# Kernel optimization log

Measured on AMD Instinct MI355X. Metric: run time of the kernel, lower is better.

## Reference

```python
import jax, jax.numpy as jnp
import numpy as np

B, T, C = 4, 2048, 2048
N_HEAD = 16
HEAD_DIM = C // N_HEAD
ROPE_BASE = 10000.0


def setup_inputs() -> dict:
    key = jax.random.key(0)
    k1, k2, k3 = jax.random.split(key, 3)
    x = jax.random.normal(k1, (B, T, C), dtype=jnp.float32)
    Wqkv = jax.random.normal(k2, (C, 3 * C), dtype=jnp.float32) * 0.02
    bqkv = jnp.zeros((3 * C,), dtype=jnp.float32)
    Wproj = jax.random.normal(k3, (C, C), dtype=jnp.float32) * 0.02
    bproj = jnp.zeros((C,), dtype=jnp.float32)
    return {"x": x, "Wqkv": Wqkv, "bqkv": bqkv, "Wproj": Wproj, "bproj": bproj}


def _rope_cos_sin(seq_len, head_dim, dtype):
    inv_freq = 1.0 / (ROPE_BASE ** (jnp.arange(0, head_dim, 2, dtype=jnp.float32) / head_dim))
    t = jnp.arange(seq_len, dtype=jnp.float32)
    freqs = jnp.einsum("i,j->ij", t, inv_freq)          # [T, D/2]
    emb = jnp.concatenate([freqs, freqs], axis=-1)       # [T, D]
    return jnp.cos(emb).astype(dtype), jnp.sin(emb).astype(dtype)


def _rotate_half(x):
    half = x.shape[-1] // 2
    x1, x2 = x[..., :half], x[..., half:]
    return jnp.concatenate([-x2, x1], axis=-1)


def reference(x, Wqkv, bqkv, Wproj, bproj):
    b, t, c = x.shape
    qkv = x @ Wqkv + bqkv                                # [B, T, 3C]
    q, k, v = jnp.split(qkv, 3, axis=-1)
    # [B, T, C] -> [B, H, T, D]
    def to_heads(u):
        return u.reshape(b, t, N_HEAD, HEAD_DIM).transpose(0, 2, 1, 3)
    q, k, v = to_heads(q), to_heads(k), to_heads(v)
    cos, sin = _rope_cos_sin(t, HEAD_DIM, x.dtype)       # [T, D]
    cos = cos[None, None]                                # [1, 1, T, D]
    sin = sin[None, None]
    q = q * cos + _rotate_half(q) * sin
    k = k * cos + _rotate_half(k) * sin
    scale = 1.0 / np.sqrt(HEAD_DIM).astype(np.float32)
    scores = jnp.einsum("bhqd,bhkd->bhqk", q, k) * scale  # [B, H, T, T]
    causal = jnp.tril(jnp.ones((t, t), dtype=bool))
    scores = jnp.where(causal[None, None], scores, jnp.finfo(scores.dtype).min)
    att = jax.nn.softmax(scores, axis=-1)
    y = jnp.einsum("bhqk,bhkd->bhqd", att, v)             # [B, H, T, D]
    y = y.transpose(0, 2, 1, 3).reshape(b, t, c)
    return y @ Wproj + bproj
```

## Files before the change

### kernel.cpp

```cpp
#include <hip/hip_runtime.h>
#include <hip/hip_bf16.h>
#include <stdint.h>
#include <math.h>

#define NB 4
#define NT 2048
#define NC 2048
#define NH 16
#define HD 128
#define BT (NB*NT)

typedef __attribute__((ext_vector_type(8))) short s16x8;
typedef __attribute__((ext_vector_type(4))) short s16x4;
typedef __attribute__((ext_vector_type(4))) float f32x4;

typedef __attribute__((address_space(1))) void as1_void;
typedef __attribute__((address_space(3))) void as3_void;

static __device__ __forceinline__ unsigned short f2bf(float f) {
  union { float f; uint32_t u; } v; v.f = f;
  return (unsigned short)((v.u + 0x7fffu + ((v.u >> 16) & 1u)) >> 16);
}
static __device__ __forceinline__ float bf2f(unsigned short u) {
  union { uint32_t u; float f; } v; v.u = ((uint32_t)u) << 16;
  return v.f;
}
static __device__ __forceinline__ void async16(unsigned short* lds, const unsigned short* g) {
  __builtin_amdgcn_global_load_lds((as1_void*)g, (as3_void*)lds, 16, 0, 0);
}
static __device__ __forceinline__ uint32_t lds_off(void* p) {
  return (uint32_t)(size_t)(as3_void*)p;
}

__global__ void k_convert_bf16(const float* __restrict__ in, unsigned short* __restrict__ out, int n8) {
  int i = blockIdx.x * blockDim.x + threadIdx.x;
  if (i >= n8) return;
  const float4* p = (const float4*)in + (size_t)i * 2;
  float4 a = p[0], b = p[1];
  union { unsigned short s[8]; uint4 u; } o;
  o.s[0] = f2bf(a.x); o.s[1] = f2bf(a.y); o.s[2] = f2bf(a.z); o.s[3] = f2bf(a.w);
  o.s[4] = f2bf(b.x); o.s[5] = f2bf(b.y); o.s[6] = f2bf(b.z); o.s[7] = f2bf(b.w);
  ((uint4*)out)[i] = o.u;
}

__global__ void k_transpose_bf16(const float* __restrict__ W, unsigned short* __restrict__ WT, int K, int N) {
  __shared__ unsigned short tile[64][65];
  const int k0 = blockIdx.y * 64, n0 = blockIdx.x * 64;
  const int t = threadIdx.x;
  const int jj = t & 63, base_i = t >> 6;
  #pragma unroll
  for (int p = 0; p < 16; ++p) {
    int i = p * 4 + base_i;
    tile[i][jj] = f2bf(W[(size_t)(k0 + i) * N + n0 + jj]);
  }
  __syncthreads();
  #pragma unroll
  for (int p = 0; p < 16; ++p) {
    int j = p * 4 + base_i;
    WT[(size_t)(n0 + j) * K + k0 + jj] = tile[jj][j];
  }
}

__global__ void k_rope(unsigned short* __restrict__ Q, unsigned short* __restrict__ Kb) {
  int idx = blockIdx.x * 256 + threadIdx.x;
  int g = idx & 7;
  int tpos = (idx >> 3) & (NT - 1);
  int bh = idx >> 14;
  size_t o = ((size_t)bh * NT + tpos) * HD + g * 8;
  s16x8 qlo = *(const s16x8*)(Q + o),  qhi = *(const s16x8*)(Q + o + 64);
  s16x8 klo = *(const s16x8*)(Kb + o), khi = *(const s16x8*)(Kb + o + 64);
  s16x8 oql, oqh, okl, okh;
  const float qs = 0.08838834764831845f * 1.4426950408889634f;
  #pragma unroll
  for (int e = 0; e < 8; ++e) {
    const int d = g * 8 + e;
    float invf = exp2f(-(float)d * 0.2076205059304602f);
    float ang = (float)tpos * invf;
    float s, c;
    __sincosf(ang, &s, &c);
    float q1 = bf2f((unsigned short)qlo[e]), q2 = bf2f((unsigned short)qhi[e]);
    float k1 = bf2f((unsigned short)klo[e]), k2 = bf2f((unsigned short)khi[e]);
    oql[e] = (short)f2bf((q1 * c - q2 * s) * qs);
    oqh[e] = (short)f2bf((q2 * c + q1 * s) * qs);
    okl[e] = (short)f2bf(k1 * c - k2 * s);
    okh[e] = (short)f2bf(k2 * c + k1 * s);
  }
  *(s16x8*)(Q + o)       = oql;
  *(s16x8*)(Q + o + 64)  = oqh;
  *(s16x8*)(Kb + o)      = okl;
  *(s16x8*)(Kb + o + 64) = okh;
}

template<int MODE>
__global__ __launch_bounds__(256, 2)
void k_gemm_bt2(const unsigned short* __restrict__ A,
                const unsigned short* __restrict__ Bt,
                const float* __restrict__ bias,
                float* __restrict__ OutF,
                unsigned short* __restrict__ Qd,
                unsigned short* __restrict__ Kd,
                unsigned short* __restrict__ Vd,
                int M, int N, int K)
{
  __shared__ __align__(16) unsigned short Al[256 * 64];
  __shared__ __align__(16) unsigned short Bl[128 * 64];
  const int t = threadIdx.x;
  const int l = t & 63;
  const int wv = t >> 6;
  const int wm = wv >> 1, wn = wv & 1;
  const int bm = blockIdx.y * 256, bn = blockIdx.x * 128;
  const int lr = l & 15, lg = l >> 4;

  f32x4 acc[8][4];
  #pragma unroll
  for (int i = 0; i < 8; ++i)
    #pragma unroll
    for (int j = 0; j < 4; ++j)
      acc[i][j] = f32x4{0.f, 0.f, 0.f, 0.f};

  for (int k0 = 0; k0 < K; k0 += 64) {
    #pragma unroll
    for (int i = 0; i < 8; ++i) {
      const int Cc = i * 256 + t;
      const int row = Cc >> 3;
      const int kc = (Cc & 7) ^ (row & 7);
      async16(&Al[(i * 256 + (t & 192)) * 8], &A[(size_t)(bm + row) * K + k0 + kc * 8]);
    }
    #pragma unroll
    for (int i = 0; i < 4; ++i) {
      const int Cc = i * 256 + t;
      const int row = Cc >> 3;
      const int kc = (Cc & 7) ^ (row & 7);
      async16(&Bl[(i * 256 + (t & 192)) * 8], &Bt[(size_t)(bn + row) * K + k0 + kc * 8]);
    }
    __syncthreads();
    #pragma unroll
    for (int kk = 0; kk < 2; ++kk) {
      s16x8 af[8], bfr[4];
      #pragma unroll
      for (int mi = 0; mi < 8; ++mi) {
        const int row = wm * 128 + mi * 16 + lr;
        const int ch = (kk * 4 + lg) ^ (row & 7);
        af[mi] = *(const s16x8*)&Al[row * 64 + ch * 8];
      }
      #pragma unroll
      for (int ni = 0; ni < 4; ++ni) {
        const int row = wn * 64 + ni * 16 + lr;
        const int ch = (kk * 4 + lg) ^ (row & 7);
        bfr[ni] = *(const s16x8*)&Bl[row * 64 + ch * 8];
      }
      __builtin_amdgcn_s_setprio(1);
      #pragma unroll
      for (int mi = 0; mi < 8; ++mi)
        #pragma unroll
        for (int ni = 0; ni < 4; ++ni)
          acc[mi][ni] = __builtin_amdgcn_mfma_f32_16x16x32_bf16(af[mi], bfr[ni], acc[mi][ni], 0, 0, 0);
      __builtin_amdgcn_s_setprio(0);
    }
    __syncthreads();
  }

  #pragma unroll
  for (int mi = 0; mi < 8; ++mi) {
    #pragma unroll
    for (int ni = 0; ni < 4; ++ni) {
      const int col = bn + wn * 64 + ni * 16 + lr;
      const float bv = bias[col];
      #pragma unroll
      for (int r = 0; r < 4; ++r) {
        const int row = bm + wm * 128 + mi * 16 + lg * 4 + r;
        const float v = acc[mi][ni][r] + bv;
        if (MODE == 1) {
          OutF[(size_t)row * N + col] = v;
        } else {
          const int which = col >> 11;
          const int cc = col & 2047;
          const int h = cc >> 7, d = cc & 127;
          const int b = row >> 11, tp = row & 2047;
          unsigned short* dst = (which == 0) ? Qd : (which == 1 ? Kd : Vd);
          dst[(((size_t)(b * NH + h)) * NT + tp) * HD + d] = f2bf(v);
        }
      }
    }
  }
}

__global__ __launch_bounds__(256, 2)
void k_attn(const unsigned short* __restrict__ Q,
            const unsigned short* __restrict__ Kg,
            const unsigned short* __restrict__ Vg,
            unsigned short* __restrict__ Yatt)
{
  __shared__ __align__(16) unsigned short Kl[2][64 * 128];
  __shared__ __align__(16) unsigned short Vl[2][64 * 128];
  const int bh = blockIdx.x;
  const int pair = blockIdx.y;
  const int b = bh >> 4, h = bh & 15;
  const int t = threadIdx.x, l = t & 63, wv = t >> 6;
  const int lr = l & 15, lg = l >> 4;
  const size_t hoff = (size_t)bh * NT * HD;
  const unsigned short* Qh = Q + hoff;
  const unsigned short* Kh = Kg + hoff;
  const unsigned short* Vh = Vg + hoff;
  const uint32_t vbase0 = lds_off(&Vl[0][0]);

  auto stageKV = [&](int buf, int kv0) {
    #pragma unroll
    for (int i = 0; i < 4; ++i) {
      const int Cc = i * 256 + t;
      {
        const int krow = Cc >> 4;
        const int kc = (Cc & 15) ^ (krow & 7);
        async16(&Kl[buf][(i * 256 + (t & 192)) * 8], &Kh[(size_t)(kv0 + krow) * HD + kc * 8]);
      }
      {
        const int S = Cc >> 3, c8 = Cc & 7;
        const int kq = S >> 3, dq = S & 7;
        const int vk = kq * 4 + (c8 >> 1), vd = dq * 16 + (c8 & 1) * 8;
        async16(&Vl[buf][(i * 256 + (t & 192)) * 8], &Vh[(size_t)(kv0 + vk) * HD + vd]);
      }
    }
  };

  #pragma unroll 1
  for (int rep = 0; rep < 2; ++rep) {
    const int qb = rep ? (31 - pair) : pair;
    const int q0w = qb * 64 + wv * 16;
    const int qrow = q0w + lr;

    __syncthreads();

    s16x8 qf[4];
    #pragma unroll
    for (int m = 0; m < 4; ++m)
      qf[m] = *(const s16x8*)(Qh + (size_t)qrow * HD + m * 32 + lg * 8);

    f32x4 yt[8];
    #pragma unroll
    for (int n = 0; n < 8; ++n) yt[n] = f32x4{0.f, 0.f, 0.f, 0.f};
    float mrun = -1e30f, lrun = 0.f;

    auto computeTile = [&](int buf, int kv0) {
      f32x4 st[4];
      __builtin_amdgcn_s_setprio(1);
      #pragma unroll
      for (int kt = 0; kt < 4; ++kt) {
        f32x4 a = f32x4{0.f, 0.f, 0.f, 0.f};
        const int krow = kt * 16 + lr;
        #pragma unroll
        for (int m = 0; m < 4; ++m) {
          const int ch = (m * 4 + lg) ^ (krow & 7);
          s16x8 kf = *(const s16x8*)&Kl[buf][krow * 128 + ch * 8];
          a = __builtin_amdgcn_mfma_f32_16x16x32_bf16(kf, qf[m], a, 0, 0, 0);
        }
        st[kt] = a;
      }
      __builtin_amdgcn_s_setprio(0);

      if (kv0 + 63 > q0w) {
        #pragma unroll
        for (int kt = 0; kt < 4; ++kt)
          #pragma unroll
          for (int r = 0; r < 4; ++r) {
            const int key = kv0 + kt * 16 + lg * 4 + r;
            if (key > qrow) st[kt][r] = -3.0e38f;
          }
      }

      float tm = -3.0e38f;
      #pragma unroll
      for (int kt = 0; kt < 4; ++kt)
        #pragma unroll
        for (int r = 0; r < 4; ++r) tm = fmaxf(tm, st[kt][r]);
      tm = fmaxf(tm, __shfl_xor(tm, 16));
      tm = fmaxf(tm, __shfl_xor(tm, 32));
      if (!__all(tm - mrun <= 8.0f)) {
        const float mnew = fmaxf(mrun, tm);
        const float fsc = exp2f(mrun - mnew);
        mrun = mnew;
        lrun *= fsc;
        #pragma unroll
        for (int n = 0; n < 8; ++n)
          #pragma unroll
          for (int r = 0; r < 4; ++r) yt[n][r] *= fsc;
      }

      float pv[16];
      float psum = 0.f;
      #pragma unroll
      for (int kt = 0; kt < 4; ++kt)
        #pragma unroll
        for (int r = 0; r < 4; ++r) {
          const float p = exp2f(st[kt][r] - mrun);
          psum += p;
          pv[kt * 4 + r] = p;
        }
      lrun += psum;

      union { uint32_t w[4]; s16x8 v; } pu[2];
      #pragma unroll
      for (int gk = 0; gk < 2; ++gk)
        #pragma unroll
        for (int w = 0; w < 4; ++w) {
          const int i0 = (gk * 2 + (w >> 1)) * 4 + (w & 1) * 2;
          asm("v_cvt_pk_bf16_f32 %0, %1, %2" : "=v"(pu[gk].w[w]) : "v"(pv[i0]), "v"(pv[i0 + 1]));
        }

      const uint32_t vb = vbase0 + (uint32_t)buf * 16384;
      #pragma unroll
      for (int gk = 0; gk < 2; ++gk) {
        s16x4 va[8], vb2[8];
        #pragma unroll
        for (int n = 0; n < 8; ++n) {
          const uint32_t a0 = vb + ((uint32_t)((gk * 8 + lg) * 8 + n)) * 128 + (uint32_t)lr * 8;
          asm volatile("ds_read_b64_tr_b16 %0, %1" : "=v"(va[n])  : "v"(a0));
          asm volatile("ds_read_b64_tr_b16 %0, %1" : "=v"(vb2[n]) : "v"(a0 + 4096));
        }
        asm volatile("s_waitcnt lgkmcnt(0)" ::: "memory");
        __builtin_amdgcn_sched_barrier(0);
        __builtin_amdgcn_s_setprio(1);
        #pragma unroll
        for (int n = 0; n < 8; ++n) {
          s16x8 vf;
          vf[0] = va[n][0];  vf[1] = va[n][1];  vf[2] = va[n][2];  vf[3] = va[n][3];
          vf[4] = vb2[n][0]; vf[5] = vb2[n][1]; vf[6] = vb2[n][2]; vf[7] = vb2[n][3];
          yt[n] = __builtin_amdgcn_mfma_f32_16x16x32_bf16(vf, pu[gk].v, yt[n], 0, 0, 0);
        }
        __builtin_amdgcn_s_setprio(0);
      }
    };

    const int nkv = qb + 1;
    stageKV(0, 0);
    asm volatile("s_waitcnt vmcnt(0)" ::: "memory");
    __syncthreads();
    int buf = 0;
    #pragma unroll 1
    for (int kv = 0; kv < nkv - 1; ++kv) {
      stageKV(buf ^ 1, (kv + 1) * 64);
      computeTile(buf, kv * 64);
      asm volatile("s_waitcnt vmcnt(0)" ::: "memory");
      __builtin_amdgcn_s_barrier();
      buf ^= 1;
    }
    computeTile(buf, (nkv - 1) * 64);

    lrun += __shfl_xor(lrun, 16);
    lrun += __shfl_xor(lrun, 32);
    const float inv = 1.f / lrun;
    unsigned short* yrow = Yatt + (size_t)(b * NT + q0w + lr) * NC + h * HD;
    #pragma unroll
    for (int n = 0; n < 8; ++n)
      #pragma unroll
      for (int r = 0; r < 4; ++r)
        yrow[n * 16 + lg * 4 + r] = f2bf(yt[n][r] * inv);
  }
}

extern "C" void kernel_launch(void* const* d_in, const int* in_sizes, int n_in,
                              void* d_out, int out_size, void* d_ws, size_t ws_size,
                              hipStream_t stream) {
  (void)in_sizes; (void)n_in; (void)out_size; (void)ws_size;
  const float* x     = (const float*)d_in[0];
  const float* Wqkv  = (const float*)d_in[1];
  const float* bqkv  = (const float*)d_in[2];
  const float* Wproj = (const float*)d_in[3];
  const float* bproj = (const float*)d_in[4];
  float* out = (float*)d_out;
  char* ws = (char*)d_ws;

  unsigned short* xb     = (unsigned short*)(ws);
  unsigned short* WqkvT  = (unsigned short*)(ws + 33554432);
  unsigned short* WprojT = (unsigned short*)(ws + 58720256);
  unsigned short* Qb     = (unsigned short*)(ws + 67108864);
  unsigned short* Kb     = (unsigned short*)(ws + 100663296);
  unsigned short* Vb     = (unsigned short*)(ws + 134217728);
  unsigned short* att    = xb;

  k_convert_bf16<<<dim3(8192), dim3(256), 0, stream>>>(x, xb, BT * NC / 8);
  k_transpose_bf16<<<dim3(96, 32), dim3(256), 0, stream>>>(Wqkv, WqkvT, NC, 3 * NC);
  k_transpose_bf16<<<dim3(32, 32), dim3(256), 0, stream>>>(Wproj, WprojT, NC, NC);
  k_gemm_bt2<0><<<dim3(48, 32), dim3(256), 0, stream>>>(xb, WqkvT, bqkv, nullptr, Qb, Kb, Vb, BT, 3 * NC, NC);
  k_rope<<<dim3(4096), dim3(256), 0, stream>>>(Qb, Kb);
  k_attn<<<dim3(64, 16), dim3(256), 0, stream>>>(Qb, Kb, Vb, att);
  k_gemm_bt2<1><<<dim3(16, 32), dim3(256), 0, stream>>>(att, WprojT, bproj, out, nullptr, nullptr, nullptr, BT, NC, NC);
}
```

Before: 438.3 us.

## Process two query sub-tiles per wave in attention and remap GEMM block order

The attention kernel now has each wave handle 32 query rows as two 16-row groups instead of one, so each K fragment read from LDS and each V transpose read feeds two MFMAs. The query tile per block doubles to 128 rows and the grid halves in y. The output store is changed to packed bf16 conversions with 8-byte writes. Separately, the GEMM kernel remaps block indices so that consecutive launched blocks are spread in strides of one eighth of the grid, likely to match the chip's XCD round-robin placement and improve L2 locality. The cost is more registers per attention wave, fewer blocks to fill the GPU, and more masked work on the diagonal tiles.

```diff
diff --git a/kernel.cpp b/kernel.cpp
--- a/kernel.cpp
+++ b/kernel.cpp
@@ -108,7 +108,11 @@
   const int l = t & 63;
   const int wv = t >> 6;
   const int wm = wv >> 1, wn = wv & 1;
-  const int bm = blockIdx.y * 256, bn = blockIdx.x * 128;
+  const int gx = gridDim.x;
+  const int lin = blockIdx.y * gx + blockIdx.x;
+  const int qch = (gx * gridDim.y) >> 3;
+  const int nid = (lin & 7) * qch + (lin >> 3);
+  const int bm = (nid / gx) * 256, bn = (nid % gx) * 128;
   const int lr = l & 15, lg = l >> 4;
 
   f32x4 acc[8][4];
@@ -224,36 +228,39 @@
 
   #pragma unroll 1
   for (int rep = 0; rep < 2; ++rep) {
-    const int qb = rep ? (31 - pair) : pair;
-    const int q0w = qb * 64 + wv * 16;
-    const int qrow = q0w + lr;
+    const int qb16 = rep ? (15 - pair) : pair;
+    const int q0w = qb16 * 128 + wv * 32;
+    const int qrowA = q0w + lr, qrowB = q0w + 16 + lr;
 
     __syncthreads();
 
-    s16x8 qf[4];
-    #pragma unroll
-    for (int m = 0; m < 4; ++m)
-      qf[m] = *(const s16x8*)(Qh + (size_t)qrow * HD + m * 32 + lg * 8);
-
-    f32x4 yt[8];
-    #pragma unroll
-    for (int n = 0; n < 8; ++n) yt[n] = f32x4{0.f, 0.f, 0.f, 0.f};
-    float mrun = -1e30f, lrun = 0.f;
+    s16x8 qfA[4], qfB[4];
+    #pragma unroll
+    for (int m = 0; m < 4; ++m) {
+      qfA[m] = *(const s16x8*)(Qh + (size_t)qrowA * HD + m * 32 + lg * 8);
+      qfB[m] = *(const s16x8*)(Qh + (size_t)qrowB * HD + m * 32 + lg * 8);
+    }
+
+    f32x4 ytA[8], ytB[8];
+    #pragma unroll
+    for (int n = 0; n < 8; ++n) { ytA[n] = f32x4{0.f,0.f,0.f,0.f}; ytB[n] = f32x4{0.f,0.f,0.f,0.f}; }
+    float mrunA = -1e30f, lrunA = 0.f, mrunB = -1e30f, lrunB = 0.f;
 
     auto computeTile = [&](int buf, int kv0) {
-      f32x4 st[4];
+      f32x4 stA[4], stB[4];
       __builtin_amdgcn_s_setprio(1);
       #pragma unroll
       for (int kt = 0; kt < 4; ++kt) {
-        f32x4 a = f32x4{0.f, 0.f, 0.f, 0.f};
+        f32x4 a = f32x4{0.f,0.f,0.f,0.f}, bq = f32x4{0.f,0.f,0.f,0.f};
         const int krow = kt * 16 + lr;
         #pragma unroll
         for (int m = 0; m < 4; ++m) {
           const int ch = (m * 4 + lg) ^ (krow & 7);
           s16x8 kf = *(const s16x8*)&Kl[buf][krow * 128 + ch * 8];
-          a = __builtin_amdgcn_mfma_f32_16x16x32_bf16(kf, qf[m], a, 0, 0, 0);
-        }
-        st[kt] = a;
+          a  = __builtin_amdgcn_mfma_f32_16x16x32_bf16(kf, qfA[m], a, 0, 0, 0);
+          bq = __builtin_amdgcn_mfma_f32_16x16x32_bf16(kf, qfB[m], bq, 0, 0, 0);
+        }
+        stA[kt] = a; stB[kt] = bq;
       }
       __builtin_amdgcn_s_setprio(0);
 
@@ -263,47 +270,50 @@
           #pragma unroll
           for (int r = 0; r < 4; ++r) {
             const int key = kv0 + kt * 16 + lg * 4 + r;
-            if (key > qrow) st[kt][r] = -3.0e38f;
+            if (key > qrowA) stA[kt][r] = -3.0e38f;
+            if (key > qrowB) stB[kt][r] = -3.0e38f;
           }
       }
 
-      float tm = -3.0e38f;
+      float tmA = -3.0e38f, tmB = -3.0e38f;
       #pragma unroll
       for (int kt = 0; kt < 4; ++kt)
         #pragma unroll
-        for (int r = 0; r < 4; ++r) tm = fmaxf(tm, st[kt][r]);
-      tm = fmaxf(tm, __shfl_xor(tm, 16));
-      tm = fmaxf(tm, __shfl_xor(tm, 32));
-      if (!__all(tm - mrun <= 8.0f)) {
-        const float mnew = fmaxf(mrun, tm);
-        const float fsc = exp2f(mrun - mnew);
-        mrun = mnew;
-        lrun *= fsc;
+        for (int r = 0; r < 4; ++r) { tmA = fmaxf(tmA, stA[kt][r]); tmB = fmaxf(tmB, stB[kt][r]); }
+      tmA = fmaxf(tmA, __shfl_xor(tmA, 16)); tmA = fmaxf(tmA, __shfl_xor(tmA, 32));
+      tmB = fmaxf(tmB, __shfl_xor(tmB, 16)); tmB = fmaxf(tmB, __shfl_xor(tmB, 32));
+      if (!__all((tmA - mrunA <= 8.0f) && (tmB - mrunB <= 8.0f))) {
+        const float mnA = fmaxf(mrunA, tmA), mnB = fmaxf(mrunB, tmB);
+        const float fsA = exp2f(mrunA - mnA), fsB = exp2f(mrunB - mnB);
+        mrunA = mnA; mrunB = mnB;
+        lrunA *= fsA; lrunB *= fsB;
         #pragma unroll
         for (int n = 0; n < 8; ++n)
           #pragma unroll
-          for (int r = 0; r < 4; ++r) yt[n][r] *= fsc;
-      }
-
-      float pv[16];
-      float psum = 0.f;
+          for (int r = 0; r < 4; ++r) { ytA[n][r] *= fsA; ytB[n][r] *= fsB; }
+      }
+
+      float pvA[16], pvB[16];
+      float psA = 0.f, psB = 0.f;
       #pragma unroll
       for (int kt = 0; kt < 4; ++kt)
         #pragma unroll
         for (int r = 0; r < 4; ++r) {
-          const float p = exp2f(st[kt][r] - mrun);
-          psum += p;
-          pv[kt * 4 + r] = p;
-        }
-      lrun += psum;
-
-      union { uint32_t w[4]; s16x8 v; } pu[2];
+          const float pa = exp2f(stA[kt][r] - mrunA);
+          const float pb = exp2f(stB[kt][r] - mrunB);
+          psA += pa; psB += pb;
+          pvA[kt * 4 + r] = pa; pvB[kt * 4 + r] = pb;
+        }
+      lrunA += psA; lrunB += psB;
+
+      union { uint32_t w[4]; s16x8 v; } puA[2], puB[2];
       #pragma unroll
       for (int gk = 0; gk < 2; ++gk)
         #pragma unroll
         for (int w = 0; w < 4; ++w) {
           const int i0 = (gk * 2 + (w >> 1)) * 4 + (w & 1) * 2;
-          asm("v_cvt_pk_bf16_f32 %0, %1, %2" : "=v"(pu[gk].w[w]) : "v"(pv[i0]), "v"(pv[i0 + 1]));
+          asm("v_cvt_pk_bf16_f32 %0, %1, %2" : "=v"(puA[gk].w[w]) : "v"(pvA[i0]), "v"(pvA[i0 + 1]));
+          asm("v_cvt_pk_bf16_f32 %0, %1, %2" : "=v"(puB[gk].w[w]) : "v"(pvB[i0]), "v"(pvB[i0 + 1]));
         }
 
       const uint32_t vb = vbase0 + (uint32_t)buf * 16384;
@@ -324,13 +334,14 @@
           s16x8 vf;
           vf[0] = va[n][0];  vf[1] = va[n][1];  vf[2] = va[n][2];  vf[3] = va[n][3];
           vf[4] = vb2[n][0]; vf[5] = vb2[n][1]; vf[6] = vb2[n][2]; vf[7] = vb2[n][3];
-          yt[n] = __builtin_amdgcn_mfma_f32_16x16x32_bf16(vf, pu[gk].v, yt[n], 0, 0, 0);
+          ytA[n] = __builtin_amdgcn_mfma_f32_16x16x32_bf16(vf, puA[gk].v, ytA[n], 0, 0, 0);
+          ytB[n] = __builtin_amdgcn_mfma_f32_16x16x32_bf16(vf, puB[gk].v, ytB[n], 0, 0, 0);
         }
         __builtin_amdgcn_s_setprio(0);
       }
     };
 
-    const int nkv = qb + 1;
+    const int nkv = 2 * qb16 + 2;
     stageKV(0, 0);
     asm volatile("s_waitcnt vmcnt(0)" ::: "memory");
     __syncthreads();
@@ -345,15 +356,23 @@
     }
     computeTile(buf, (nkv - 1) * 64);
 
-    lrun += __shfl_xor(lrun, 16);
-    lrun += __shfl_xor(lrun, 32);
-    const float inv = 1.f / lrun;
-    unsigned short* yrow = Yatt + (size_t)(b * NT + q0w + lr) * NC + h * HD;
-    #pragma unroll
-    for (int n = 0; n < 8; ++n)
-      #pragma unroll
-      for (int r = 0; r < 4; ++r)
-        yrow[n * 16 + lg * 4 + r] = f2bf(yt[n][r] * inv);
+    lrunA += __shfl_xor(lrunA, 16); lrunA += __shfl_xor(lrunA, 32);
+    lrunB += __shfl_xor(lrunB, 16); lrunB += __shfl_xor(lrunB, 32);
+    const float invA = 1.f / lrunA, invB = 1.f / lrunB;
+    unsigned short* yrowA = Yatt + (size_t)(b * NT + qrowA) * NC + h * HD;
+    unsigned short* yrowB = Yatt + (size_t)(b * NT + qrowB) * NC + h * HD;
+    #pragma unroll
+    for (int n = 0; n < 8; ++n) {
+      uint32_t u0, u1;
+      asm("v_cvt_pk_bf16_f32 %0, %1, %2" : "=v"(u0) : "v"(ytA[n][0] * invA), "v"(ytA[n][1] * invA));
+      asm("v_cvt_pk_bf16_f32 %0, %1, %2" : "=v"(u1) : "v"(ytA[n][2] * invA), "v"(ytA[n][3] * invA));
+      uint2 pk; pk.x = u0; pk.y = u1;
+      *(uint2*)(yrowA + n * 16 + lg * 4) = pk;
+      asm("v_cvt_pk_bf16_f32 %0, %1, %2" : "=v"(u0) : "v"(ytB[n][0] * invB), "v"(ytB[n][1] * invB));
+      asm("v_cvt_pk_bf16_f32 %0, %1, %2" : "=v"(u1) : "v"(ytB[n][2] * invB), "v"(ytB[n][3] * invB));
+      pk.x = u0; pk.y = u1;
+      *(uint2*)(yrowB + n * 16 + lg * 4) = pk;
+    }
   }
 }
 
@@ -382,6 +401,6 @@
   k_transpose_bf16<<<dim3(32, 32), dim3(256), 0, stream>>>(Wproj, WprojT, NC, NC);
   k_gemm_bt2<0><<<dim3(48, 32), dim3(256), 0, stream>>>(xb, WqkvT, bqkv, nullptr, Qb, Kb, Vb, BT, 3 * NC, NC);
   k_rope<<<dim3(4096), dim3(256), 0, stream>>>(Qb, Kb);
-  k_attn<<<dim3(64, 16), dim3(256), 0, stream>>>(Qb, Kb, Vb, att);
+  k_attn<<<dim3(64, 8), dim3(256), 0, stream>>>(Qb, Kb, Vb, att);
   k_gemm_bt2<1><<<dim3(16, 32), dim3(256), 0, stream>>>(att, WprojT, bproj, out, nullptr, nullptr, nullptr, BT, NC, NC);
 }
```

After: 413.8 us. -5.6%, faster.
